# Kernel optimization log

Measured on AMD Instinct MI355X. Metric: run time of the kernel, lower is better.

The kernel has to match this reference:

```python
import jax, jax.numpy as jnp
import numpy as np

S = 14
L_COORD = 5.0
L_NOOBJ = 0.5


def setup_inputs() -> dict:
    key = jax.random.key(0)
    k1, k2, k3, k4 = jax.random.split(key, 4)
    N = 4096
    # positive uniforms so sqrt(w), sqrt(h) and IoU areas are well-defined (as in real YOLO outputs)
    pred_tensor = jax.random.uniform(k1, (N, S, S, 30), dtype=jnp.float32, minval=0.01, maxval=1.0)
    target_boxes = jax.random.uniform(k2, (N, S, S, 4), dtype=jnp.float32, minval=0.01, maxval=1.0)
    target_cls = jax.random.uniform(k3, (N, S, S, 20), dtype=jnp.float32)
    has_object_map = jax.random.bernoulli(k4, 0.15, (N, S, S))
    return {"pred_tensor": pred_tensor, "target_boxes": target_boxes,
            "target_cls": target_cls, "has_object_map": has_object_map}


def _xywh2xyxy(b):
    # b: (..., 4) as [cx, cy, w, h]; cx,cy are in grid units -> divide by S
    x, y, w, h = b[..., 0], b[..., 1], b[..., 2], b[..., 3]
    return jnp.stack([x / S - 0.5 * w, y / S - 0.5 * h,
                      x / S + 0.5 * w, y / S + 0.5 * h], axis=-1)


def _iou_pairwise(b1, b2):
    # elementwise IoU between matched boxes (diag of compute_iou), b: (..., 4) xyxy
    lt = jnp.maximum(b1[..., :2], b2[..., :2])
    rb = jnp.minimum(b1[..., 2:], b2[..., 2:])
    wh = jnp.maximum(rb - lt, 0.0)
    inter = wh[..., 0] * wh[..., 1]
    a1 = (b1[..., 2] - b1[..., 0]) * (b1[..., 3] - b1[..., 1])
    a2 = (b2[..., 2] - b2[..., 0]) * (b2[..., 3] - b2[..., 1])
    return inter / (a1 + a2 - inter)


def reference(pred_tensor, target_boxes, target_cls, has_object_map):
    N = pred_tensor.shape[0]
    obj = has_object_map.astype(pred_tensor.dtype)          # (N,S,S)
    noobj = 1.0 - obj

    box1 = pred_tensor[..., 0:5]
    box2 = pred_tensor[..., 5:10]
    pred_cls = pred_tensor[..., 10:]

    # class loss: masked sum-MSE over object cells
    cls_loss = jnp.sum(obj[..., None] * (pred_cls - target_cls) ** 2)

    # no-object loss: confidences of both predictors in non-object cells vs 0
    no_obj_loss = L_NOOBJ * jnp.sum(noobj * (box1[..., 4] ** 2 + box2[..., 4] ** 2))

    # best-of-B selection by IoU against target (elementwise, matched per cell)
    tgt_xyxy = _xywh2xyxy(target_boxes)
    iou1 = _iou_pairwise(_xywh2xyxy(box1[..., :4]), tgt_xyxy)
    iou2 = _iou_pairwise(_xywh2xyxy(box2[..., :4]), tgt_xyxy)
    take1 = iou1 > iou2
    best_iou = jnp.where(take1, iou1, iou2)                  # (N,S,S)
    best_box = jnp.where(take1[..., None], box1, box2)       # (N,S,S,5)

    xy_err = jnp.sum((best_box[..., :2] - target_boxes[..., :2]) ** 2, axis=-1)
    wh_err = jnp.sum((jnp.sqrt(best_box[..., 2:4]) - jnp.sqrt(target_boxes[..., 2:4])) ** 2, axis=-1)
    reg_loss = L_COORD * jnp.sum(obj * (xy_err + wh_err))

    # containing-object confidence loss; target IoU is detached
    contain_loss = jnp.sum(obj * (best_box[..., 4] - jax.lax.stop_gradient(best_iou)) ** 2)

    total = cls_loss + no_obj_loss + contain_loss + reg_loss
    # [total, reg, containing_obj, no_obj, cls], each averaged over batch
    return jnp.stack([total, reg_loss, contain_loss, no_obj_loss, cls_loss]) / N
```

## Files before the change

### kernel.cpp

```cpp
#include <hip/hip_runtime.h>


#define CELLS   802816
#define THREADS 256
#define NBLK    1024
#define NWAVES  (NBLK * 4)
#define CHUNK   32
#define CHUNKS  (CELLS / CHUNK)
#define MAXSLOT 7
#define L_COORD 5.0f
#define L_NOOBJ 0.5f

#define ISSUE(cn, opk, P, T, Bx) do {                                         \
    const float4* t4_ = (const float4*)tcls + (size_t)(cn) * 160;             \
    const float4* p4_ = (const float4*)pred + (size_t)(cn) * 240;             \
    T[0] = t4_[((opk) & 1) ? lane : 0];                                       \
    T[1] = t4_[((opk) & 2) ? i1 : 0];                                         \
    if (lane < 32) T[2] = t4_[((opk) & 4) ? i2 : 0];                          \
    Bx = ((const float4*)tbox)[(size_t)(cn) * CHUNK + (((opk) & 8) ? bcell : 0)]; \
    P[0] = p4_[lane]; P[1] = p4_[i1]; P[2] = p4_[i2];                         \
    if (lane < 48) P[3] = p4_[lane + 192];                                    \
  } while (0)

#define STAGE(P) do {                                                         \
    s4[lane] = P[0]; s4[i1] = P[1]; s4[i2] = P[2];                            \
    if (lane < 48) s4[lane + 192] = P[3];                                     \
  } while (0)

#define COMPUTE(opk, T, Bx) do {                                              \
    float cl_ = 0.f;                                                          \
    if ((opk) & 1) {                                                          \
      const float2 a_ = *(const float2*)&seg[cc0 * 30 + 10 + ch0];            \
      const float2 b_ = *(const float2*)&seg[cc0 * 30 + 12 + ch0];            \
      float d0_ = a_.x - T[0].x, d1_ = a_.y - T[0].y;                         \
      float d2_ = b_.x - T[0].z, d3_ = b_.y - T[0].w;                         \
      cl_ += d0_*d0_ + d1_*d1_ + d2_*d2_ + d3_*d3_;                           \
    }                                                                         \
    if ((opk) & 2) {                                                          \
      const float2 a_ = *(const float2*)&seg[cc1 * 30 + 10 + ch1];            \
      const float2 b_ = *(const float2*)&seg[cc1 * 30 + 12 + ch1];            \
      float d0_ = a_.x - T[1].x, d1_ = a_.y - T[1].y;                         \
      float d2_ = b_.x - T[1].z, d3_ = b_.y - T[1].w;                         \
      cl_ += d0_*d0_ + d1_*d1_ + d2_*d2_ + d3_*d3_;                           \
    }                                                                         \
    if ((lane < 32) && ((opk) & 4)) {                                         \
      const float2 a_ = *(const float2*)&seg[cc2 * 30 + 10 + ch2];            \
      const float2 b_ = *(const float2*)&seg[cc2 * 30 + 12 + ch2];            \
      float d0_ = a_.x - T[2].x, d1_ = a_.y - T[2].y;                         \
      float d2_ = b_.x - T[2].z, d3_ = b_.y - T[2].w;                         \
      cl_ += d0_*d0_ + d1_*d1_ + d2_*d2_ + d3_*d3_;                           \
    }                                                                         \
    acc_cls += cl_;                                                           \
    const float* pp_ = &seg[bcell * 30 + box * 5];                            \
    float x_ = pp_[0], y_ = pp_[1], w_ = pp_[2], h_ = pp_[3], cf_ = pp_[4];   \
    const bool ox_ = ((opk) & 8) != 0;                                        \
    if (!ox_) acc_noobj += cf_ * cf_;                                         \
    float txc_ = Bx.x * invS, tyc_ = Bx.y * invS;                             \
    float tx1_ = txc_ - 0.5f * Bx.z, ty1_ = tyc_ - 0.5f * Bx.w;               \
    float tx2_ = txc_ + 0.5f * Bx.z, ty2_ = tyc_ + 0.5f * Bx.w;               \
    float ta_  = (tx2_ - tx1_) * (ty2_ - ty1_);                               \
    float ax1_ = x_ * invS - 0.5f * w_, ay1_ = y_ * invS - 0.5f * h_;         \
    float ax2_ = x_ * invS + 0.5f * w_, ay2_ = y_ * invS + 0.5f * h_;         \
    float a1_  = (ax2_ - ax1_) * (ay2_ - ay1_);                               \
    float iw_  = fmaxf(fminf(ax2_, tx2_) - fmaxf(ax1_, tx1_), 0.f);           \
    float ih_  = fmaxf(fminf(ay2_, ty2_) - fmaxf(ay1_, ty1_), 0.f);           \
    float in_  = iw_ * ih_;                                                   \
    float iou_ = in_ / (a1_ + ta_ - in_);                                     \
    float iouo_ = __shfl_xor(iou_, 1);                                        \
    bool win_ = (box == 0) ? (iou_ > iouo_) : !(iouo_ > iou_);                \
    if (win_ && ox_) {                                                        \
      float dx_ = x_ - Bx.x, dy_ = y_ - Bx.y;                                 \
      float dw_ = sqrtf(w_) - sqrtf(Bx.z);                                    \
      float dh_ = sqrtf(h_) - sqrtf(Bx.w);                                    \
      acc_reg  += dx_*dx_ + dy_*dy_ + dw_*dw_ + dh_*dh_;                      \
      float dc_ = cf_ - iou_;                                                 \
      acc_cont += dc_ * dc_;                                                  \
    }                                                                         \
  } while (0)

#define SLOT(s, PX, TX, BX, PY, TY, BY) do {                                  \
    const int c_ = w0 + (s) * NWAVES;                                         \
    if (c_ < CHUNKS) {                                                        \
      STAGE(PX);                                                              \
      __builtin_amdgcn_sched_barrier(0);                                      \
      const int cn_ = c_ + NWAVES;                                            \
      if (cn_ < CHUNKS) ISSUE(cn_, opack[(s) + 1], PY, TY, BY);               \
      __builtin_amdgcn_sched_barrier(0);                                      \
      COMPUTE(opack[(s)], TX, BX);                                            \
    }                                                                         \
  } while (0)

__global__ __launch_bounds__(THREADS, 4) void yolo_main(
    const float* __restrict__ pred,
    const float* __restrict__ tbox,
    const float* __restrict__ tcls,
    const int*   __restrict__ objmap,
    float4*      __restrict__ part)
{
    __shared__ float lds[4 * 960];
    __shared__ float red[4][4];

    const int tid  = threadIdx.x;
    const int wv   = tid >> 6;
    const int lane = tid & 63;
    float*  seg = &lds[wv * 960];
    float4* s4  = (float4*)seg;

    const int cc0 = lane / 5,   ch0 = (lane - cc0 * 5) * 4;
    const int i1  = lane + 64;
    const int cc1 = i1 / 5,     ch1 = (i1 - cc1 * 5) * 4;
    const int i2  = lane + 128;
    const int cc2 = (lane < 32) ? (i2 / 5) : 0;
    const int ch2 = (lane < 32) ? (i2 - cc2 * 5) * 4 : 0;
    const int bcell = lane >> 1;
    const int box   = lane & 1;
    const float invS = 1.0f / 14.0f;

    float acc_reg = 0.f, acc_cont = 0.f, acc_noobj = 0.f, acc_cls = 0.f;

    const int w0 = blockIdx.x * 4 + wv;

    int opack[MAXSLOT + 1];
    #pragma unroll
    for (int s = 0; s < MAXSLOT; ++s) {
        const int c = w0 + s * NWAVES;
        int v = 0;
        if (c < CHUNKS) {
            const int* ob = objmap + (size_t)c * CHUNK;
            v  = ob[cc0]  ? 1 : 0;
            v |= ob[cc1]  ? 2 : 0;
            v |= ob[cc2]  ? 4 : 0;
            v |= ob[bcell]? 8 : 0;
        }
        opack[s] = v;
    }
    opack[MAXSLOT] = 0;

    float4 PA[4], TA[3], BA;
    float4 PB[4], TB[3], BB;

    ISSUE(w0, opack[0], PA, TA, BA);
    __builtin_amdgcn_sched_barrier(0);

    SLOT(0, PA, TA, BA, PB, TB, BB);
    SLOT(1, PB, TB, BB, PA, TA, BA);
    SLOT(2, PA, TA, BA, PB, TB, BB);
    SLOT(3, PB, TB, BB, PA, TA, BA);
    SLOT(4, PA, TA, BA, PB, TB, BB);
    SLOT(5, PB, TB, BB, PA, TA, BA);
    SLOT(6, PA, TA, BA, PB, TB, BB);

    #pragma unroll
    for (int off = 32; off > 0; off >>= 1) {
        acc_reg   += __shfl_down(acc_reg,   off);
        acc_cont  += __shfl_down(acc_cont,  off);
        acc_noobj += __shfl_down(acc_noobj, off);
        acc_cls   += __shfl_down(acc_cls,   off);
    }
    if (lane == 0) {
        red[wv][0] = acc_reg;
        red[wv][1] = acc_cont;
        red[wv][2] = acc_noobj;
        red[wv][3] = acc_cls;
    }
    __syncthreads();
    if (tid == 0) {
        float4 p;
        p.x = red[0][0] + red[1][0] + red[2][0] + red[3][0];
        p.y = red[0][1] + red[1][1] + red[2][1] + red[3][1];
        p.z = red[0][2] + red[1][2] + red[2][2] + red[3][2];
        p.w = red[0][3] + red[1][3] + red[2][3] + red[3][3];
        part[blockIdx.x] = p;
    }
}

__global__ __launch_bounds__(1024) void yolo_reduce(
    const float4* __restrict__ part, float* __restrict__ out)
{
    __shared__ float red[16][4];
    float r = 0.f, c = 0.f, n = 0.f, cl = 0.f;
    for (int i = threadIdx.x; i < NBLK; i += 1024) {
        float4 p = part[i];
        r += p.x; c += p.y; n += p.z; cl += p.w;
    }
    #pragma unroll
    for (int off = 32; off > 0; off >>= 1) {
        r  += __shfl_down(r,  off);
        c  += __shfl_down(c,  off);
        n  += __shfl_down(n,  off);
        cl += __shfl_down(cl, off);
    }
    const int wave = threadIdx.x >> 6, lane = threadIdx.x & 63;
    if (lane == 0) {
        red[wave][0] = r; red[wave][1] = c; red[wave][2] = n; red[wave][3] = cl;
    }
    __syncthreads();
    if (threadIdx.x == 0) {
        float R = 0.f, C = 0.f, Nn = 0.f, Cl = 0.f;
        #pragma unroll
        for (int w = 0; w < 16; ++w) {
            R += red[w][0]; C += red[w][1]; Nn += red[w][2]; Cl += red[w][3];
        }
        const float invN = 1.0f / 4096.0f;
        float reg   = L_COORD * R  * invN;
        float cont  =           C  * invN;
        float noobj = L_NOOBJ * Nn * invN;
        float cls   =           Cl * invN;
        out[0] = reg + cont + noobj + cls;
        out[1] = reg;
        out[2] = cont;
        out[3] = noobj;
        out[4] = cls;
    }
}

extern "C" void kernel_launch(void* const* d_in, const int* in_sizes, int n_in,
                              void* d_out, int out_size, void* d_ws, size_t ws_size,
                              hipStream_t stream) {
    const float* pred   = (const float*)d_in[0];
    const float* tbox   = (const float*)d_in[1];
    const float* tcls   = (const float*)d_in[2];
    const int*   objmap = (const int*)  d_in[3];
    float4* part = (float4*)d_ws;
    float*  out  = (float*)d_out;

    yolo_main<<<NBLK, THREADS, 0, stream>>>(pred, tbox, tcls, objmap, part);
    yolo_reduce<<<1, 1024, 0, stream>>>(part, out);
}
```

Before: 214.1 us.

## Load pred chunks straight into LDS with double-buffered global_load_lds

Replaces the register-staged copy of prediction chunks into shared memory with direct global-to-LDS loads into two alternating per-wave buffers. Target loads become inline-asm dwordx4 loads, and explicit vmcnt waits keep the next chunk in flight while the current one is computed. This removes the VGPR round trip and the LDS store instructions. In exchange LDS use doubles and launch bounds drop to 2 blocks per CU. Correctness rests on hand-counted vmcnt values, which is fragile; lanes 48-63 issue only 7 loads, and there is no barrier ordering LDS reads against reuse of the buffer.

```diff
diff --git a/kernel.cpp b/kernel.cpp
--- a/kernel.cpp
+++ b/kernel.cpp
@@ -11,47 +11,58 @@
 #define L_COORD 5.0f
 #define L_NOOBJ 0.5f
 
-#define ISSUE(cn, opk, P, T, Bx) do {                                         \
-    const float4* t4_ = (const float4*)tcls + (size_t)(cn) * 160;             \
-    const float4* p4_ = (const float4*)pred + (size_t)(cn) * 240;             \
-    T[0] = t4_[((opk) & 1) ? lane : 0];                                       \
-    T[1] = t4_[((opk) & 2) ? i1 : 0];                                         \
-    if (lane < 32) T[2] = t4_[((opk) & 4) ? i2 : 0];                          \
-    Bx = ((const float4*)tbox)[(size_t)(cn) * CHUNK + (((opk) & 8) ? bcell : 0)]; \
-    P[0] = p4_[lane]; P[1] = p4_[i1]; P[2] = p4_[i2];                         \
-    if (lane < 48) P[3] = p4_[lane + 192];                                    \
+typedef float f32x4 __attribute__((ext_vector_type(4)));
+
+#define GL16(gsrc, ldst)                                                      \
+    __builtin_amdgcn_global_load_lds(                                         \
+        (const __attribute__((address_space(1))) void*)(gsrc),                \
+        (__attribute__((address_space(3))) void*)(ldst), 16, 0, 0)
+
+#define ALOAD16(dst, ptr)                                                     \
+    asm volatile("global_load_dwordx4 %0, %1, off" : "=v"(dst) : "v"(ptr))
+
+#define WAIT8  asm volatile("s_waitcnt vmcnt(8)" ::: "memory")
+#define WAIT0  asm volatile("s_waitcnt vmcnt(0)" ::: "memory")
+
+#define ISSUE(cn, opk, T0, T1, T2, Bx, bufn) do {                             \
+    const f32x4* p4_ = (const f32x4*)pred + (size_t)(cn) * 240;               \
+    const f32x4* t4_ = (const f32x4*)tcls + (size_t)(cn) * 160;               \
+    GL16(p4_ + lane,       (bufn));                                           \
+    GL16(p4_ + 64 + lane,  (bufn) + 256);                                     \
+    GL16(p4_ + 128 + lane, (bufn) + 512);                                     \
+    if (lane < 48) GL16(p4_ + 192 + lane, (bufn) + 768);                      \
+    ALOAD16(T0, t4_ + (((opk) & 1) ? lane : 0));                              \
+    ALOAD16(T1, t4_ + (((opk) & 2) ? i1 : 0));                                \
+    ALOAD16(T2, t4_ + ((((opk) & 4) && lane < 32) ? i2 : 0));                 \
+    ALOAD16(Bx, (const f32x4*)tbox + (size_t)(cn) * CHUNK +                   \
+                (((opk) & 8) ? bcell : 0));                                   \
   } while (0)
 
-#define STAGE(P) do {                                                         \
-    s4[lane] = P[0]; s4[i1] = P[1]; s4[i2] = P[2];                            \
-    if (lane < 48) s4[lane + 192] = P[3];                                     \
-  } while (0)
-
-#define COMPUTE(opk, T, Bx) do {                                              \
+#define COMPUTE(opk, T0, T1, T2, Bx, sg) do {                                 \
     float cl_ = 0.f;                                                          \
     if ((opk) & 1) {                                                          \
-      const float2 a_ = *(const float2*)&seg[cc0 * 30 + 10 + ch0];            \
-      const float2 b_ = *(const float2*)&seg[cc0 * 30 + 12 + ch0];            \
-      float d0_ = a_.x - T[0].x, d1_ = a_.y - T[0].y;                         \
-      float d2_ = b_.x - T[0].z, d3_ = b_.y - T[0].w;                         \
+      const float2 a_ = *(const float2*)&(sg)[cc0 * 30 + 10 + ch0];           \
+      const float2 b_ = *(const float2*)&(sg)[cc0 * 30 + 12 + ch0];           \
+      float d0_ = a_.x - T0.x, d1_ = a_.y - T0.y;                             \
+      float d2_ = b_.x - T0.z, d3_ = b_.y - T0.w;                             \
       cl_ += d0_*d0_ + d1_*d1_ + d2_*d2_ + d3_*d3_;                           \
     }                                                                         \
     if ((opk) & 2) {                                                          \
-      const float2 a_ = *(const float2*)&seg[cc1 * 30 + 10 + ch1];            \
-      const float2 b_ = *(const float2*)&seg[cc1 * 30 + 12 + ch1];            \
-      float d0_ = a_.x - T[1].x, d1_ = a_.y - T[1].y;                         \
-      float d2_ = b_.x - T[1].z, d3_ = b_.y - T[1].w;                         \
+      const float2 a_ = *(const float2*)&(sg)[cc1 * 30 + 10 + ch1];           \
+      const float2 b_ = *(const float2*)&(sg)[cc1 * 30 + 12 + ch1];           \
+      float d0_ = a_.x - T1.x, d1_ = a_.y - T1.y;                             \
+      float d2_ = b_.x - T1.z, d3_ = b_.y - T1.w;                             \
       cl_ += d0_*d0_ + d1_*d1_ + d2_*d2_ + d3_*d3_;                           \
     }                                                                         \
     if ((lane < 32) && ((opk) & 4)) {                                         \
-      const float2 a_ = *(const float2*)&seg[cc2 * 30 + 10 + ch2];            \
-      const float2 b_ = *(const float2*)&seg[cc2 * 30 + 12 + ch2];            \
-      float d0_ = a_.x - T[2].x, d1_ = a_.y - T[2].y;                         \
-      float d2_ = b_.x - T[2].z, d3_ = b_.y - T[2].w;                         \
+      const float2 a_ = *(const float2*)&(sg)[cc2 * 30 + 10 + ch2];           \
+      const float2 b_ = *(const float2*)&(sg)[cc2 * 30 + 12 + ch2];           \
+      float d0_ = a_.x - T2.x, d1_ = a_.y - T2.y;                             \
+      float d2_ = b_.x - T2.z, d3_ = b_.y - T2.w;                             \
       cl_ += d0_*d0_ + d1_*d1_ + d2_*d2_ + d3_*d3_;                           \
     }                                                                         \
     acc_cls += cl_;                                                           \
-    const float* pp_ = &seg[bcell * 30 + box * 5];                            \
+    const float* pp_ = &(sg)[bcell * 30 + box * 5];                           \
     float x_ = pp_[0], y_ = pp_[1], w_ = pp_[2], h_ = pp_[3], cf_ = pp_[4];   \
     const bool ox_ = ((opk) & 8) != 0;                                        \
     if (!ox_) acc_noobj += cf_ * cf_;                                         \
@@ -78,33 +89,36 @@
     }                                                                         \
   } while (0)
 
-#define SLOT(s, PX, TX, BX, PY, TY, BY) do {                                  \
+#define SLOT(s, T0c,T1c,T2c,Bc, T0n,T1n,T2n,Bn, bufc, bufn) do {              \
     const int c_ = w0 + (s) * NWAVES;                                         \
     if (c_ < CHUNKS) {                                                        \
-      STAGE(PX);                                                              \
+      const int cn_ = c_ + NWAVES;                                            \
+      if (cn_ < CHUNKS) {                                                     \
+        ISSUE(cn_, opack[(s) + 1], T0n, T1n, T2n, Bn, bufn);                  \
+        WAIT8;                                                                \
+      } else {                                                                \
+        WAIT0;                                                                \
+      }                                                                       \
       __builtin_amdgcn_sched_barrier(0);                                      \
-      const int cn_ = c_ + NWAVES;                                            \
-      if (cn_ < CHUNKS) ISSUE(cn_, opack[(s) + 1], PY, TY, BY);               \
-      __builtin_amdgcn_sched_barrier(0);                                      \
-      COMPUTE(opack[(s)], TX, BX);                                            \
+      COMPUTE(opack[(s)], T0c, T1c, T2c, Bc, bufc);                           \
     }                                                                         \
   } while (0)
 
-__global__ __launch_bounds__(THREADS, 4) void yolo_main(
+__global__ __launch_bounds__(THREADS, 2) void yolo_main(
     const float* __restrict__ pred,
     const float* __restrict__ tbox,
     const float* __restrict__ tcls,
     const int*   __restrict__ objmap,
     float4*      __restrict__ part)
 {
-    __shared__ float lds[4 * 960];
+    __shared__ float lds[4 * 1920];
     __shared__ float red[4][4];
 
     const int tid  = threadIdx.x;
     const int wv   = tid >> 6;
     const int lane = tid & 63;
-    float*  seg = &lds[wv * 960];
-    float4* s4  = (float4*)seg;
+    float* buf0 = &lds[wv * 1920];
+    float* buf1 = buf0 + 960;
 
     const int cc0 = lane / 5,   ch0 = (lane - cc0 * 5) * 4;
     const int i1  = lane + 64;
@@ -136,19 +150,19 @@
     }
     opack[MAXSLOT] = 0;
 
-    float4 PA[4], TA[3], BA;
-    float4 PB[4], TB[3], BB;
-
-    ISSUE(w0, opack[0], PA, TA, BA);
+    f32x4 TA0, TA1, TA2, BA;
+    f32x4 TB0, TB1, TB2, BB;
+
+    ISSUE(w0, opack[0], TA0, TA1, TA2, BA, buf0);
     __builtin_amdgcn_sched_barrier(0);
 
-    SLOT(0, PA, TA, BA, PB, TB, BB);
-    SLOT(1, PB, TB, BB, PA, TA, BA);
-    SLOT(2, PA, TA, BA, PB, TB, BB);
-    SLOT(3, PB, TB, BB, PA, TA, BA);
-    SLOT(4, PA, TA, BA, PB, TB, BB);
-    SLOT(5, PB, TB, BB, PA, TA, BA);
-    SLOT(6, PA, TA, BA, PB, TB, BB);
+    SLOT(0, TA0,TA1,TA2,BA, TB0,TB1,TB2,BB, buf0, buf1);
+    SLOT(1, TB0,TB1,TB2,BB, TA0,TA1,TA2,BA, buf1, buf0);
+    SLOT(2, TA0,TA1,TA2,BA, TB0,TB1,TB2,BB, buf0, buf1);
+    SLOT(3, TB0,TB1,TB2,BB, TA0,TA1,TA2,BA, buf1, buf0);
+    SLOT(4, TA0,TA1,TA2,BA, TB0,TB1,TB2,BB, buf0, buf1);
+    SLOT(5, TB0,TB1,TB2,BB, TA0,TA1,TA2,BA, buf1, buf0);
+    SLOT(6, TA0,TA1,TA2,BA, TB0,TB1,TB2,BB, buf0, buf1);
 
     #pragma unroll
     for (int off = 32; off > 0; off >>= 1) {
```

Result: faster. 198.6 us (-7.2%).
